# Optimization experiments

Hardware: AMD Instinct MI355X
Metric: run time of the kernel (lower is better)

Reference implementation:

```python
import jax, jax.numpy as jnp
import numpy as np

VOCAB, EMBED, HIDDEN = 50000, 256, 512
B, SEQ = 64, 200


def setup_inputs() -> dict:
    key = jax.random.key(0)
    ks = jax.random.split(key, 16)
    h2 = 2 * HIDDEN
    inp = {
        "input_idx": jax.random.randint(ks[0], (B,), 0, VOCAB),
        "encoded": jax.random.normal(ks[1], (B, SEQ, h2), jnp.float32),
        "encoded_idx": jax.random.randint(ks[2], (B, SEQ), 0, VOCAB),
        "prev_state": jax.random.normal(ks[3], (B, HIDDEN), jnp.float32),
        "weighted": jax.random.normal(ks[4], (B, 1, h2), jnp.float32),
        "order": 1,
        # learned parameters
        "embed_table": jax.random.normal(ks[5], (VOCAB, EMBED), jnp.float32) * 0.02,
        "w_ih": jax.random.normal(ks[6], (3 * HIDDEN, EMBED + h2), jnp.float32) * 0.02,
        "w_hh": jax.random.normal(ks[7], (3 * HIDDEN, HIDDEN), jnp.float32) * 0.02,
        "b_ih": jax.random.normal(ks[8], (3 * HIDDEN,), jnp.float32) * 0.02,
        "b_hh": jax.random.normal(ks[9], (3 * HIDDEN,), jnp.float32) * 0.02,
        "wo_w": jax.random.normal(ks[10], (VOCAB, HIDDEN), jnp.float32) * 0.02,
        "wo_b": jax.random.normal(ks[11], (VOCAB,), jnp.float32) * 0.02,
        "wc_w": jax.random.normal(ks[12], (HIDDEN, h2), jnp.float32) * 0.02,
        "wc_b": jax.random.normal(ks[13], (HIDDEN,), jnp.float32) * 0.02,
    }
    return inp


def _gru_step(x, h, w_ih, w_hh, b_ih, b_hh):
    # torch GRU gate ordering: reset, update, new
    gx = x @ w_ih.T + b_ih            # [b, 3h]
    gh = h @ w_hh.T + b_hh            # [b, 3h]
    xr, xz, xn = jnp.split(gx, 3, axis=-1)
    hr, hz, hn = jnp.split(gh, 3, axis=-1)
    r = jax.nn.sigmoid(xr + hr)
    z = jax.nn.sigmoid(xz + hz)
    n = jnp.tanh(xn + r * hn)
    return (1.0 - z) * n + z * h


def reference(input_idx, encoded, encoded_idx, prev_state, weighted, order,
              embed_table, w_ih, w_hh, b_ih, b_hh, wo_w, wo_b, wc_w, wc_b):
    b, seq, _ = encoded.shape
    vocab = wo_w.shape[0]

    # GRU single step on [embed(input); weighted]
    x = jnp.concatenate([embed_table[input_idx], weighted[:, 0, :]], axis=-1)
    state = _gru_step(x, prev_state, w_ih, w_hh, b_ih, b_hh)  # [b, h]

    # generate score over vocab
    score_g = state @ wo_w.T + wo_b                           # [b, vocab]

    # copy score over source positions
    score_c = jnp.tanh(jnp.einsum('bsk,hk->bsh', encoded, wc_w) + wc_b)
    score_c = jnp.einsum('bsh,bh->bs', score_c, state)        # [b, seq]

    encoded_mask = (encoded_idx != 0).astype(score_c.dtype)
    idx_from_input = (encoded_idx == input_idx[:, None]).astype(score_c.dtype)
    score_c = score_c * encoded_mask * idx_from_input

    # joint softmax over [vocab + seq]
    probs = jax.nn.softmax(jnp.concatenate([score_g, score_c], axis=1), axis=1)
    prob_g = probs[:, :vocab]
    prob_c = probs[:, vocab:]                                 # [b, seq]

    # scatter copy probs into vocab space (equivalent to one-hot bmm)
    flat_idx = (jnp.arange(b)[:, None] * vocab + encoded_idx).reshape(-1)
    prob_c_to_g = jnp.zeros((b * vocab,), probs.dtype).at[flat_idx].add(
        prob_c.reshape(-1)).reshape(b, vocab)

    out = (prob_g + prob_c_to_g)[:, None, :]                  # [b, 1, vocab]

    # selective-read attention, renormalized where sum > 0 (detached divisor)
    attn = prob_c * idx_from_input
    s = jax.lax.stop_gradient(jnp.sum(attn, axis=1, keepdims=True))
    attn = jnp.where(s > 0.0, attn / jnp.where(s > 0.0, s, 1.0), attn)
    weighted_new = jnp.einsum('bs,bsk->bk', attn, encoded)[:, None, :]  # [b,1,2h]

    return out, state, weighted_new
```

## Files before the change

kernel.cpp:

```cpp
#include <hip/hip_runtime.h>
#include <hip/hip_bf16.h>
#include <cstdint>
#include <cstddef>

#define VOCAB  50000
#define EMBED  256
#define HIDDEN 512
#define BATCH  64
#define SEQ    200
#define H2     1024
#define XDIM   1280
#define G3     1536
#define V4     (VOCAB/4)
#define NVB    782
#define NVBP   784
#define NFB    13
#define NHS    8
#define NSCC   (BATCH*NHS)

typedef __attribute__((ext_vector_type(8))) short short8;
typedef __attribute__((ext_vector_type(4))) float f32x4;

__device__ __forceinline__ short f2bf(float f) {
  uint32_t u = __builtin_bit_cast(uint32_t, f);
  uint32_t r = (u + 0x7fffu + ((u >> 16) & 1u)) >> 16;
  return (short)(r & 0xffffu);
}

__device__ __forceinline__ short8 pack8(float4 v0, float4 v1) {
  short8 fr;
  fr[0]=f2bf(v0.x); fr[1]=f2bf(v0.y); fr[2]=f2bf(v0.z); fr[3]=f2bf(v0.w);
  fr[4]=f2bf(v1.x); fr[5]=f2bf(v1.y); fr[6]=f2bf(v1.z); fr[7]=f2bf(v1.w);
  return fr;
}

__launch_bounds__(256)
__global__ void gru_gemm(const int* __restrict__ idx, const float* __restrict__ embed,
                         const float* __restrict__ weighted, const float* __restrict__ h0,
                         const float* __restrict__ w_ih, const float* __restrict__ w_hh,
                         float* __restrict__ gxp, float* __restrict__ ghp) {
  __shared__ __align__(16) short As[4 * 64 * 8];
  const int tid  = threadIdx.x;
  const int wave = tid >> 6, lane = tid & 63;
  const int l15  = lane & 15, lk = lane >> 4;
  const int slice = blockIdx.y;
  const bool isX  = slice < 8;
  const float* B  = isX ? w_ih : w_hh;
  const int ldb   = isX ? XDIM : HIDDEN;
  const int kbeg  = isX ? slice * 160 : (slice - 8) * 128;
  const int kend  = kbeg + (isX ? 160 : 128);
  float* C = isX ? (gxp + (size_t)slice * BATCH * G3)
                 : (ghp + (size_t)(slice - 8) * BATCH * G3);
  const int ncol = blockIdx.x * 64 + wave * 16;

  f32x4 acc0 = {0,0,0,0}, acc1 = {0,0,0,0}, acc2 = {0,0,0,0}, acc3 = {0,0,0,0};

  const int sl  = tid & 63;
  const int sm  = (tid >> 6) * 16 + (sl & 15);
  const int skb = (sl >> 4) * 8;

  const int nrow = ncol + l15;
  const float* Bbase = B + (size_t)nrow * ldb + lk * 8;

  for (int kc = kbeg; kc < kend; kc += 32) {
    {
      const float4* ap;
      if (isX) {
        int col = kc + skb;
        if (col < EMBED) ap = reinterpret_cast<const float4*>(embed + (size_t)idx[sm] * EMBED + col);
        else             ap = reinterpret_cast<const float4*>(weighted + (size_t)sm * H2 + (col - EMBED));
      } else {
        ap = reinterpret_cast<const float4*>(h0 + (size_t)sm * HIDDEN + kc + skb);
      }
      *reinterpret_cast<short8*>(&As[tid * 8]) = pack8(ap[0], ap[1]);
    }
    __syncthreads();
    short8 bf;
    {
      const float4* bp = reinterpret_cast<const float4*>(Bbase + kc);
      bf = pack8(bp[0], bp[1]);
    }
    short8 a0 = *reinterpret_cast<const short8*>(&As[(0*64 + lane)*8]);
    short8 a1 = *reinterpret_cast<const short8*>(&As[(1*64 + lane)*8]);
    short8 a2 = *reinterpret_cast<const short8*>(&As[(2*64 + lane)*8]);
    short8 a3 = *reinterpret_cast<const short8*>(&As[(3*64 + lane)*8]);
    acc0 = __builtin_amdgcn_mfma_f32_16x16x32_bf16(a0, bf, acc0, 0, 0, 0);
    acc1 = __builtin_amdgcn_mfma_f32_16x16x32_bf16(a1, bf, acc1, 0, 0, 0);
    acc2 = __builtin_amdgcn_mfma_f32_16x16x32_bf16(a2, bf, acc2, 0, 0, 0);
    acc3 = __builtin_amdgcn_mfma_f32_16x16x32_bf16(a3, bf, acc3, 0, 0, 0);
    __syncthreads();
  }

  const int n = ncol + l15;
  #pragma unroll
  for (int r = 0; r < 4; ++r) {
    C[(size_t)(0*16 + lk*4 + r) * G3 + n] = acc0[r];
    C[(size_t)(1*16 + lk*4 + r) * G3 + n] = acc1[r];
    C[(size_t)(2*16 + lk*4 + r) * G3 + n] = acc2[r];
    C[(size_t)(3*16 + lk*4 + r) * G3 + n] = acc3[r];
  }
}

__launch_bounds__(256)
__global__ void gru_gates(const float* __restrict__ gxp, const float* __restrict__ ghp,
                          const float* __restrict__ b_ih, const float* __restrict__ b_hh,
                          const float* __restrict__ h0, float* __restrict__ out_state,
                          unsigned short* __restrict__ stateF) {
  int i = blockIdx.x * 256 + threadIdx.x;
  int b = i >> 9, h = i & 511;
  float xr = b_ih[h], xz = b_ih[HIDDEN + h], xn = b_ih[2*HIDDEN + h];
  #pragma unroll
  for (int s = 0; s < 8; ++s) {
    const float* g = gxp + (size_t)s * BATCH * G3 + (size_t)b * G3;
    xr += g[h]; xz += g[HIDDEN + h]; xn += g[2*HIDDEN + h];
  }
  float hr = b_hh[h], hz = b_hh[HIDDEN + h], hn = b_hh[2*HIDDEN + h];
  #pragma unroll
  for (int s = 0; s < 4; ++s) {
    const float* g = ghp + (size_t)s * BATCH * G3 + (size_t)b * G3;
    hr += g[h]; hz += g[HIDDEN + h]; hn += g[2*HIDDEN + h];
  }
  float r = 1.f / (1.f + __expf(-(xr + hr)));
  float z = 1.f / (1.f + __expf(-(xz + hz)));
  float n = tanhf(xn + r * hn);
  float st = (1.f - z) * n + z * h0[(size_t)b*HIDDEN + h];
  out_state[(size_t)b*HIDDEN + h] = st;
  int fi = ((h >> 5) * 4 + (b >> 4)) * 512 + ((b & 15) + 16 * ((h >> 3) & 3)) * 8 + (h & 7);
  stateF[fi] = (unsigned short)f2bf(st);
}

__launch_bounds__(256)
__global__ void vocab_v5(const unsigned short* __restrict__ stateF,
                         const float* __restrict__ state,
                         const float* __restrict__ wo_w, const float* __restrict__ wo_b,
                         const int* __restrict__ eidx, const int* __restrict__ iidx,
                         const float* __restrict__ enc, const float* __restrict__ wc_w,
                         const float* __restrict__ wc_b,
                         float* __restrict__ E, float* __restrict__ sccp,
                         float* __restrict__ Spart) {
  __shared__ float red[256];
  __shared__ int   act[SEQ];
  const int bid = blockIdx.x;
  const int tid = threadIdx.x;

  if (bid < NSCC) {
    const int b  = bid >> 3, hs = bid & 7;
    const int in0 = iidx[b];
    if (tid < SEQ) {
      int e = eidx[b*SEQ + tid];
      act[tid] = (e != 0 && e == in0);
      sccp[(size_t)(b*SEQ + tid)*NHS + hs] = 0.f;
    }
    __syncthreads();
    const int hl = tid >> 2, kq = tid & 3;
    const int h  = hs*64 + hl;
    const float4* wr = reinterpret_cast<const float4*>(wc_w + (size_t)h*H2) + kq*64;
    const float  sh  = state[(size_t)b*HIDDEN + h];
    const float  bh  = wc_b[h];
    for (int sq = 0; sq < SEQ; ++sq) {
      if (act[sq]) {
        const float4* er = reinterpret_cast<const float4*>(enc + (size_t)b*SEQ*H2 + (size_t)sq*H2) + kq*64;
        float d = 0.f;
        #pragma unroll 8
        for (int k = 0; k < 64; ++k) {
          float4 a = er[k], w = wr[k];
          d += a.x*w.x + a.y*w.y + a.z*w.z + a.w*w.w;
        }
        d += __shfl_xor(d, 1);
        d += __shfl_xor(d, 2);
        float ph = (kq == 0) ? tanhf(d + bh) * sh : 0.f;
        red[tid] = ph;
        __syncthreads();
        for (int off = 128; off > 0; off >>= 1) {
          if (tid < off) red[tid] += red[tid + off];
          __syncthreads();
        }
        if (tid == 0) sccp[(size_t)(b*SEQ + sq)*NHS + hs] = red[0];
        __syncthreads();
      }
    }
    return;
  }

  const int vb   = bid - NSCC;
  const int wave = tid >> 6, lane = tid & 63;
  const int l15  = lane & 15, lk = lane >> 4;
  const int ncol = vb * 64 + wave * 16;
  int nrow = ncol + l15; if (nrow > VOCAB - 1) nrow = VOCAB - 1;
  const float*  Bb = wo_w + (size_t)nrow * HIDDEN + lk * 8;
  const short8* Af = reinterpret_cast<const short8*>(stateF);

  f32x4 acc0 = {0,0,0,0}, acc1 = {0,0,0,0}, acc2 = {0,0,0,0}, acc3 = {0,0,0,0};
  #pragma unroll 4
  for (int c = 0; c < 16; ++c) {
    const float4* bp = reinterpret_cast<const float4*>(Bb + c*32);
    float4 b0 = bp[0], b1 = bp[1];
    short8 a0 = Af[(c*4 + 0)*64 + lane];
    short8 a1 = Af[(c*4 + 1)*64 + lane];
    short8 a2 = Af[(c*4 + 2)*64 + lane];
    short8 a3 = Af[(c*4 + 3)*64 + lane];
    short8 bf = pack8(b0, b1);
    acc0 = __builtin_amdgcn_mfma_f32_16x16x32_bf16(a0, bf, acc0, 0, 0, 0);
    acc1 = __builtin_amdgcn_mfma_f32_16x16x32_bf16(a1, bf, acc1, 0, 0, 0);
    acc2 = __builtin_amdgcn_mfma_f32_16x16x32_bf16(a2, bf, acc2, 0, 0, 0);
    acc3 = __builtin_amdgcn_mfma_f32_16x16x32_bf16(a3, bf, acc3, 0, 0, 0);
  }

  const int n = ncol + l15;
  const bool valid = n < VOCAB;
  const float bv = valid ? wo_b[n] : 0.f;
  f32x4 accs[4] = {acc0, acc1, acc2, acc3};
  #pragma unroll
  for (int a = 0; a < 4; ++a) {
    #pragma unroll
    for (int r = 0; r < 4; ++r) {
      float ev = valid ? __expf(accs[a][r] + bv) : 0.f;
      if (valid) E[(size_t)(a*16 + lk*4 + r) * VOCAB + n] = ev;
      float v = ev;
      v += __shfl_xor(v, 1); v += __shfl_xor(v, 2);
      v += __shfl_xor(v, 4); v += __shfl_xor(v, 8);
      if (l15 == 0) red[wave*64 + a*16 + lk*4 + r] = v;
    }
  }
  __syncthreads();
  if (tid < 64)
    Spart[(size_t)tid * NVBP + vb] =
        red[0*64+tid] + red[1*64+tid] + red[2*64+tid] + red[3*64+tid];
}

__launch_bounds__(256)
__global__ void finalize_fused(const int* __restrict__ eidx, const int* __restrict__ iidx,
                               const float* __restrict__ sccp, const float* __restrict__ Spart,
                               const float* __restrict__ enc,
                               float* __restrict__ out0, float* __restrict__ wnew) {
  const int bid = blockIdx.x;
  const int tid = threadIdx.x;

  if (bid < BATCH) {
    __shared__ float attn_sh[SEQ];
    __shared__ float fnorm_sh;
    const int b = bid;
    const int in0 = iidx[b];
    if (tid < SEQ) {
      float sc = 0.f;
      #pragma unroll
      for (int hs = 0; hs < NHS; ++hs) sc += sccp[(size_t)(b*SEQ + tid)*NHS + hs];
      int e = eidx[b*SEQ + tid];
      attn_sh[tid] = (e == in0) ? __expf(sc) : 0.f;
    }
    __syncthreads();
    if (tid == 0) {
      float s = 0.f;
      for (int i = 0; i < SEQ; ++i) s += attn_sh[i];
      fnorm_sh = (s > 0.f) ? 1.f / s : 1.f;
    }
    __syncthreads();
    const float f = fnorm_sh;
    float a0 = 0, a1 = 0, a2 = 0, a3 = 0;
    const float4* ep = reinterpret_cast<const float4*>(enc + (size_t)b*SEQ*H2);
    for (int s = 0; s < SEQ; ++s) {
      float a = attn_sh[s];
      if (a != 0.f) {
        a *= f;
        float4 v = ep[(size_t)s*(H2/4) + tid];
        a0 += a*v.x; a1 += a*v.y; a2 += a*v.z; a3 += a*v.w;
      }
    }
    float4 o = {a0, a1, a2, a3};
    reinterpret_cast<float4*>(wnew + (size_t)b*H2)[tid] = o;
    return;
  }

  __shared__ int   me[SEQ];
  __shared__ float mp[SEQ];
  __shared__ float sred[256];
  __shared__ int   cnt;
  const int q = bid - BATCH;
  const int b = q / NFB, c = q % NFB;
  if (tid == 0) cnt = 0;
  float ps = 0.f;
  for (int i = tid; i < NVB; i += 256) ps += Spart[(size_t)b * NVBP + i];
  float ex = 0.f;
  int e = -1;
  if (tid < SEQ) {
    float sc = 0.f;
    #pragma unroll
    for (int hs = 0; hs < NHS; ++hs) sc += sccp[(size_t)(b*SEQ + tid)*NHS + hs];
    ex = __expf(sc);
    e = eidx[b*SEQ + tid];
  }
  sred[tid] = ps + ex;
  __syncthreads();
  if (tid < SEQ && (unsigned)(e - c*4096) < 4096u) {
    int j = atomicAdd(&cnt, 1);
    me[j] = e; mp[j] = ex;
  }
  for (int off = 128; off > 0; off >>= 1) {
    __syncthreads();
    if (tid < off) sred[tid] += sred[tid + off];
  }
  __syncthreads();
  const float inv = 1.f / sred[0];
  const int ncnt = cnt;
  #pragma unroll
  for (int t = 0; t < 4; ++t) {
    const int i4 = c * 1024 + t * 256 + tid;
    if (i4 < V4) {
      float4 v = reinterpret_cast<const float4*>(out0 + (size_t)b*VOCAB)[i4];
      float4 o;
      o.x = v.x * inv; o.y = v.y * inv; o.z = v.z * inv; o.w = v.w * inv;
      const int base = i4 * 4;
      for (int j = 0; j < ncnt; ++j) {
        unsigned d = (unsigned)(me[j] - base);
        if (d < 4u) (&o.x)[d] += mp[j] * inv;
      }
      reinterpret_cast<float4*>(out0 + (size_t)b*VOCAB)[i4] = o;
    }
  }
}

extern "C" void kernel_launch(void* const* d_in, const int* in_sizes, int n_in,
                              void* d_out, int out_size, void* d_ws, size_t ws_size,
                              hipStream_t stream) {
  (void)in_sizes; (void)n_in; (void)out_size; (void)ws_size;
  const int*   input_idx  = (const int*)d_in[0];
  const float* encoded    = (const float*)d_in[1];
  const int*   enc_idx    = (const int*)d_in[2];
  const float* prev_state = (const float*)d_in[3];
  const float* weighted   = (const float*)d_in[4];
  const float* embed      = (const float*)d_in[6];
  const float* w_ih       = (const float*)d_in[7];
  const float* w_hh       = (const float*)d_in[8];
  const float* b_ih       = (const float*)d_in[9];
  const float* b_hh       = (const float*)d_in[10];
  const float* wo_w       = (const float*)d_in[11];
  const float* wo_b       = (const float*)d_in[12];
  const float* wc_w       = (const float*)d_in[13];
  const float* wc_b       = (const float*)d_in[14];

  float* out0      = (float*)d_out;
  float* out_state = out0 + (size_t)BATCH * VOCAB;
  float* out_wnew  = out_state + BATCH * HIDDEN;

  float* ws    = (float*)d_ws;
  float* gxp   = ws;
  float* ghp   = ws + (size_t)8 * BATCH * G3;
  unsigned short* stateF = (unsigned short*)(ws + (size_t)12 * BATCH * G3);
  float* sccp  = ws + (size_t)12 * BATCH * G3 + 8192;
  float* Spart = sccp + (size_t)BATCH * SEQ * NHS;

  gru_gemm<<<dim3(G3/64, 12), 256, 0, stream>>>(input_idx, embed, weighted, prev_state,
                                                w_ih, w_hh, gxp, ghp);
  gru_gates<<<(BATCH*HIDDEN)/256, 256, 0, stream>>>(gxp, ghp, b_ih, b_hh, prev_state,
                                                    out_state, stateF);
  vocab_v5<<<NSCC + NVB, 256, 0, stream>>>(stateF, out_state, wo_w, wo_b,
                                           enc_idx, input_idx, encoded, wc_w, wc_b,
                                           out0, sccp, Spart);
  finalize_fused<<<BATCH + BATCH*NFB, 256, 0, stream>>>(enc_idx, input_idx, sccp, Spart,
                                                        encoded, out0, out_wnew);
}
```

Measured before the change: 82.29 us.

## Split vocab GEMM K-dimension across two wave groups with 512-thread blocks

```diff
diff --git a/kernel.cpp b/kernel.cpp
--- a/kernel.cpp
+++ b/kernel.cpp
@@ -105,7 +105,7 @@
 __global__ void gru_gates(const float* __restrict__ gxp, const float* __restrict__ ghp,
                           const float* __restrict__ b_ih, const float* __restrict__ b_hh,
                           const float* __restrict__ h0, float* __restrict__ out_state,
-                          unsigned short* __restrict__ stateF) {
+                          float* __restrict__ stateWS, unsigned short* __restrict__ stateF) {
   int i = blockIdx.x * 256 + threadIdx.x;
   int b = i >> 9, h = i & 511;
   float xr = b_ih[h], xz = b_ih[HIDDEN + h], xn = b_ih[2*HIDDEN + h];
@@ -125,21 +125,23 @@
   float n = tanhf(xn + r * hn);
   float st = (1.f - z) * n + z * h0[(size_t)b*HIDDEN + h];
   out_state[(size_t)b*HIDDEN + h] = st;
+  stateWS[(size_t)b*HIDDEN + h] = st;
   int fi = ((h >> 5) * 4 + (b >> 4)) * 512 + ((b & 15) + 16 * ((h >> 3) & 3)) * 8 + (h & 7);
   stateF[fi] = (unsigned short)f2bf(st);
 }
 
-__launch_bounds__(256)
-__global__ void vocab_v5(const unsigned short* __restrict__ stateF,
-                         const float* __restrict__ state,
+__launch_bounds__(512)
+__global__ void vocab_v7(const unsigned short* __restrict__ stateF,
+                         const float* __restrict__ stateWS,
                          const float* __restrict__ wo_w, const float* __restrict__ wo_b,
                          const int* __restrict__ eidx, const int* __restrict__ iidx,
                          const float* __restrict__ enc, const float* __restrict__ wc_w,
                          const float* __restrict__ wc_b,
                          float* __restrict__ E, float* __restrict__ sccp,
                          float* __restrict__ Spart) {
-  __shared__ float red[256];
+  __shared__ float red[512];
   __shared__ int   act[SEQ];
+  __shared__ __align__(16) f32x4 LDSX[16][64];
   const int bid = blockIdx.x;
   const int tid = threadIdx.x;
 
@@ -152,26 +154,27 @@
       sccp[(size_t)(b*SEQ + tid)*NHS + hs] = 0.f;
     }
     __syncthreads();
-    const int hl = tid >> 2, kq = tid & 3;
+    const int hl = tid >> 3, kq = tid & 7;
     const int h  = hs*64 + hl;
-    const float4* wr = reinterpret_cast<const float4*>(wc_w + (size_t)h*H2) + kq*64;
-    const float  sh  = state[(size_t)b*HIDDEN + h];
+    const float4* wr = reinterpret_cast<const float4*>(wc_w + (size_t)h*H2) + kq*32;
+    const float  sh  = stateWS[(size_t)b*HIDDEN + h];
     const float  bh  = wc_b[h];
     for (int sq = 0; sq < SEQ; ++sq) {
       if (act[sq]) {
-        const float4* er = reinterpret_cast<const float4*>(enc + (size_t)b*SEQ*H2 + (size_t)sq*H2) + kq*64;
+        const float4* er = reinterpret_cast<const float4*>(enc + (size_t)b*SEQ*H2 + (size_t)sq*H2) + kq*32;
         float d = 0.f;
         #pragma unroll 8
-        for (int k = 0; k < 64; ++k) {
+        for (int k = 0; k < 32; ++k) {
           float4 a = er[k], w = wr[k];
           d += a.x*w.x + a.y*w.y + a.z*w.z + a.w*w.w;
         }
         d += __shfl_xor(d, 1);
         d += __shfl_xor(d, 2);
+        d += __shfl_xor(d, 4);
         float ph = (kq == 0) ? tanhf(d + bh) * sh : 0.f;
         red[tid] = ph;
         __syncthreads();
-        for (int off = 128; off > 0; off >>= 1) {
+        for (int off = 256; off > 0; off >>= 1) {
           if (tid < off) red[tid] += red[tid + off];
           __syncthreads();
         }
@@ -184,15 +187,18 @@
 
   const int vb   = bid - NSCC;
   const int wave = tid >> 6, lane = tid & 63;
+  const int w4   = wave & 3, kw = wave >> 2;
   const int l15  = lane & 15, lk = lane >> 4;
-  const int ncol = vb * 64 + wave * 16;
+  const int ncol = vb * 64 + w4 * 16;
   int nrow = ncol + l15; if (nrow > VOCAB - 1) nrow = VOCAB - 1;
   const float*  Bb = wo_w + (size_t)nrow * HIDDEN + lk * 8;
   const short8* Af = reinterpret_cast<const short8*>(stateF);
 
   f32x4 acc0 = {0,0,0,0}, acc1 = {0,0,0,0}, acc2 = {0,0,0,0}, acc3 = {0,0,0,0};
+  const int c0 = kw * 8;
   #pragma unroll 4
-  for (int c = 0; c < 16; ++c) {
+  for (int cc = 0; cc < 8; ++cc) {
+    const int c = c0 + cc;
     const float4* bp = reinterpret_cast<const float4*>(Bb + c*32);
     float4 b0 = bp[0], b1 = bp[1];
     short8 a0 = Af[(c*4 + 0)*64 + lane];
@@ -206,20 +212,34 @@
     acc3 = __builtin_amdgcn_mfma_f32_16x16x32_bf16(a3, bf, acc3, 0, 0, 0);
   }
 
-  const int n = ncol + l15;
-  const bool valid = n < VOCAB;
-  const float bv = valid ? wo_b[n] : 0.f;
-  f32x4 accs[4] = {acc0, acc1, acc2, acc3};
-  #pragma unroll
-  for (int a = 0; a < 4; ++a) {
+  if (kw == 1) {
+    LDSX[0*4 + w4][lane] = acc0;
+    LDSX[1*4 + w4][lane] = acc1;
+    LDSX[2*4 + w4][lane] = acc2;
+    LDSX[3*4 + w4][lane] = acc3;
+  }
+  __syncthreads();
+  if (kw == 0) {
+    acc0 += LDSX[0*4 + w4][lane];
+    acc1 += LDSX[1*4 + w4][lane];
+    acc2 += LDSX[2*4 + w4][lane];
+    acc3 += LDSX[3*4 + w4][lane];
+
+    const int n = ncol + l15;
+    const bool valid = n < VOCAB;
+    const float bv = valid ? wo_b[n] : 0.f;
+    f32x4 accs[4] = {acc0, acc1, acc2, acc3};
     #pragma unroll
-    for (int r = 0; r < 4; ++r) {
-      float ev = valid ? __expf(accs[a][r] + bv) : 0.f;
-      if (valid) E[(size_t)(a*16 + lk*4 + r) * VOCAB + n] = ev;
-      float v = ev;
-      v += __shfl_xor(v, 1); v += __shfl_xor(v, 2);
-      v += __shfl_xor(v, 4); v += __shfl_xor(v, 8);
-      if (l15 == 0) red[wave*64 + a*16 + lk*4 + r] = v;
+    for (int a = 0; a < 4; ++a) {
+      #pragma unroll
+      for (int r = 0; r < 4; ++r) {
+        float ev = valid ? __expf(accs[a][r] + bv) : 0.f;
+        if (valid) E[(size_t)(a*16 + lk*4 + r) * VOCAB + n] = ev;
+        float v = ev;
+        v += __shfl_xor(v, 1); v += __shfl_xor(v, 2);
+        v += __shfl_xor(v, 4); v += __shfl_xor(v, 8);
+        if (l15 == 0) red[w4*64 + a*16 + lk*4 + r] = v;
+      }
     }
   }
   __syncthreads();
@@ -342,18 +362,19 @@
   float* out_state = out0 + (size_t)BATCH * VOCAB;
   float* out_wnew  = out_state + BATCH * HIDDEN;
 
-  float* ws    = (float*)d_ws;
-  float* gxp   = ws;
-  float* ghp   = ws + (size_t)8 * BATCH * G3;
+  float* ws     = (float*)d_ws;
+  float* gxp    = ws;
+  float* ghp    = ws + (size_t)8 * BATCH * G3;
   unsigned short* stateF = (unsigned short*)(ws + (size_t)12 * BATCH * G3);
-  float* sccp  = ws + (size_t)12 * BATCH * G3 + 8192;
-  float* Spart = sccp + (size_t)BATCH * SEQ * NHS;
+  float* stateWS= ws + (size_t)12 * BATCH * G3 + 16384;
+  float* sccp   = stateWS + BATCH * HIDDEN;
+  float* Spart  = sccp + (size_t)BATCH * SEQ * NHS;
 
   gru_gemm<<<dim3(G3/64, 12), 256, 0, stream>>>(input_idx, embed, weighted, prev_state,
                                                 w_ih, w_hh, gxp, ghp);
   gru_gates<<<(BATCH*HIDDEN)/256, 256, 0, stream>>>(gxp, ghp, b_ih, b_hh, prev_state,
-                                                    out_state, stateF);
-  vocab_v5<<<NSCC + NVB, 256, 0, stream>>>(stateF, out_state, wo_w, wo_b,
+                                                    out_state, stateWS, stateF);
+  vocab_v7<<<NSCC + NVB, 512, 0, stream>>>(stateF, stateWS, wo_w, wo_b,
                                            enc_idx, input_idx, encoded, wc_w, wc_b,
                                            out0, sccp, Spart);
   finalize_fused<<<BATCH + BATCH*NFB, 256, 0, stream>>>(enc_idx, input_idx, sccp, Spart,
```

After: 98.42 us. 1.2x slower.
